# Kernel optimization log

Measured on AMD Instinct MI355X. Metric: run time of the kernel, lower is better.

## Reference

```python
import jax, jax.numpy as jnp
import numpy as np

ALPHA = 0.2  # leaky relu slope
NEG_BIG = -9000000000000000.0


def setup_inputs() -> dict:
    key = jax.random.key(0)
    k1, k2, k3, k4 = jax.random.split(key, 4)
    B, N, Fin, Fout = 8, 2048, 256, 256
    h = jax.random.normal(k1, (B, N, Fin), dtype=jnp.float32)
    adj = jax.random.randint(k2, (B, N, N), 0, 2, dtype=jnp.int32)
    # xavier_uniform with gain=1.414
    gain = 1.414
    limW = gain * np.sqrt(6.0 / (Fin + Fout))
    W = jax.random.uniform(k3, (Fin, Fout), dtype=jnp.float32, minval=-limW, maxval=limW)
    lima = gain * np.sqrt(6.0 / (2 * Fout + 1))
    a = jax.random.uniform(k4, (2 * Fout, 1), dtype=jnp.float32, minval=-lima, maxval=lima)
    return {"h": h, "adj": adj, "W": W, "a": a}


def reference(h, adj, W, a):
    # Wh: [B, N, F]
    Wh = jnp.matmul(h, W)
    Fout = W.shape[1]
    a1 = a[:Fout, 0]   # scores for source node i (repeat_interleave side)
    a2 = a[Fout:, 0]   # scores for target node j (repeat side)
    # e[b,i,j] = leakyrelu(Wh[b,i]@a1 + Wh[b,j]@a2)  -- decomposed, no O(N^2 * 2F) tensor
    s1 = jnp.einsum('bnf,f->bn', Wh, a1)  # [B, N]
    s2 = jnp.einsum('bnf,f->bn', Wh, a2)  # [B, N]
    e = jax.nn.leaky_relu(s1[:, :, None] + s2[:, None, :], negative_slope=ALPHA)
    masked = jnp.where(adj > 0, e, jnp.full_like(e, NEG_BIG))
    attention = jax.nn.softmax(masked, axis=2)  # dropout=0 (eval mode)
    h_prime = jnp.matmul(attention, Wh)  # [B, N, F]
    return jax.nn.elu(h_prime)
```

## Files before the change

kernel.cpp:

```cpp
#include <hip/hip_runtime.h>

typedef __attribute__((ext_vector_type(8))) short bhalf8;
typedef __attribute__((ext_vector_type(4))) float floatx4;

#define ALPHA_LR 0.2f

__device__ __forceinline__ unsigned short f2bf(float f) {
  union { float f; unsigned int u; } v; v.f = f;
  unsigned int r = v.u + 0x7fffu + ((v.u >> 16) & 1u);
  return (unsigned short)(r >> 16);
}
__device__ __forceinline__ float bf2f(unsigned short u) {
  union { unsigned int u; float f; } v; v.u = ((unsigned int)u) << 16;
  return v.f;
}
__device__ __forceinline__ void gld16(const void* g, void* l) {
  __builtin_amdgcn_global_load_lds((const __attribute__((address_space(1))) unsigned int*)g,
                                   (__attribute__((address_space(3))) unsigned int*)l,
                                   16, 0, 0);
}

__global__ void k0w_split(const float* __restrict__ W,
                          unsigned short* __restrict__ WThi,
                          unsigned short* __restrict__ WTlo) {
  __shared__ float s[16][17];
  const int tx = threadIdx.x, ty = threadIdx.y;
  const int n0 = blockIdx.x * 16, k0 = blockIdx.y * 16;
  s[ty][tx] = W[(k0 + ty) * 256 + n0 + tx];
  __syncthreads();
  float v = s[tx][ty];
  const int k = k0 + tx, n = n0 + ty;
  unsigned short hi = f2bf(v);
  unsigned short lo = f2bf(v - bf2f(hi));
  const int idx = (k >> 5) * 8192 + n * 32 + (k & 31);
  WThi[idx] = hi;
  WTlo[idx] = lo;
}

__global__ __launch_bounds__(512, 2) void k1_mfma(const float* __restrict__ h,
                                                  const unsigned short* __restrict__ Bhi_g,
                                                  const unsigned short* __restrict__ Blo_g,
                                                  const float* __restrict__ a_g,
                                                  unsigned short* __restrict__ WhPack,
                                                  float* __restrict__ s1,
                                                  float* __restrict__ s2) {
  __shared__ unsigned short Ah[64 * 264], Al[64 * 264];
  __shared__ unsigned short Bh[2][8192], Bl[2][8192];
  __shared__ float s1red[64], s2red[64];
  const int t = threadIdx.x;
  const long r0 = (long)blockIdx.x * 64;
  const int wave = t >> 6, lane = t & 63;

  if (t < 64) { s1red[t] = 0.f; s2red[t] = 0.f; }

#pragma unroll
  for (int rep = 0; rep < 2; rep++) {
    const int off = wave * 1024 + rep * 512;
    gld16(Bhi_g + off + lane * 8, &Bh[0][off]);
    gld16(Blo_g + off + lane * 8, &Bl[0][off]);
  }

#pragma unroll
  for (int q = 0; q < 8; q++) {
    int idx = q * 512 + t;
    int row = idx >> 6, c4 = idx & 63;
    float4 x = *(const float4*)(h + (r0 + row) * 256 + c4 * 4);
    float xs[4] = {x.x, x.y, x.z, x.w};
    unsigned short hs[4], ls[4];
#pragma unroll
    for (int qq = 0; qq < 4; qq++) {
      hs[qq] = f2bf(xs[qq]);
      ls[qq] = f2bf(xs[qq] - bf2f(hs[qq]));
    }
    *(ushort4*)&Ah[row * 264 + c4 * 4] = (ushort4){hs[0], hs[1], hs[2], hs[3]};
    *(ushort4*)&Al[row * 264 + c4 * 4] = (ushort4){ls[0], ls[1], ls[2], ls[3]};
  }
  __syncthreads();

  const int wm = wave >> 2, wn = wave & 3;
  const int lhi = lane >> 4, llo = lane & 15;

  floatx4 acc[2][4];
#pragma unroll
  for (int mt = 0; mt < 2; mt++)
#pragma unroll
    for (int nt = 0; nt < 4; nt++) acc[mt][nt] = (floatx4){0.f, 0.f, 0.f, 0.f};

  for (int ks = 0; ks < 8; ks++) {
    const int cur = ks & 1, nxt = cur ^ 1, ksn = (ks + 1) & 7;
#pragma unroll
    for (int rep = 0; rep < 2; rep++) {
      const int off = wave * 1024 + rep * 512;
      gld16(Bhi_g + ksn * 8192 + off + lane * 8, &Bh[nxt][off]);
      gld16(Blo_g + ksn * 8192 + off + lane * 8, &Bl[nxt][off]);
    }

    const int k0 = ks * 32;
    bhalf8 ah[2], al[2], bh[4], bl[4];
#pragma unroll
    for (int mt = 0; mt < 2; mt++) {
      int ro = (wm * 32 + mt * 16 + llo) * 264 + k0 + lhi * 8;
      ah[mt] = *(const bhalf8*)&Ah[ro];
      al[mt] = *(const bhalf8*)&Al[ro];
    }
#pragma unroll
    for (int nt = 0; nt < 4; nt++) {
      int ro = (wn * 64 + nt * 16 + llo) * 32 + lhi * 8;
      bh[nt] = *(const bhalf8*)&Bh[cur][ro];
      bl[nt] = *(const bhalf8*)&Bl[cur][ro];
    }
#pragma unroll
    for (int mt = 0; mt < 2; mt++)
#pragma unroll
      for (int nt = 0; nt < 4; nt++) {
        acc[mt][nt] = __builtin_amdgcn_mfma_f32_16x16x32_bf16(ah[mt], bh[nt], acc[mt][nt], 0, 0, 0);
        acc[mt][nt] = __builtin_amdgcn_mfma_f32_16x16x32_bf16(ah[mt], bl[nt], acc[mt][nt], 0, 0, 0);
        acc[mt][nt] = __builtin_amdgcn_mfma_f32_16x16x32_bf16(al[mt], bh[nt], acc[mt][nt], 0, 0, 0);
      }
    __syncthreads();
  }

  float a1v[4], a2v[4];
#pragma unroll
  for (int nt = 0; nt < 4; nt++) {
    int f = wn * 64 + nt * 16 + llo;
    a1v[nt] = a_g[f];
    a2v[nt] = a_g[256 + f];
  }

  const int b = (int)(r0 >> 11);
  const int jt_base = (int)((r0 & 2047) >> 5);

#pragma unroll
  for (int mt = 0; mt < 2; mt++) {
    float p1[4], p2[4];
#pragma unroll
    for (int reg = 0; reg < 4; reg++) {
      p1[reg] = acc[mt][0][reg] * a1v[0] + acc[mt][1][reg] * a1v[1] +
                acc[mt][2][reg] * a1v[2] + acc[mt][3][reg] * a1v[3];
      p2[reg] = acc[mt][0][reg] * a2v[0] + acc[mt][1][reg] * a2v[1] +
                acc[mt][2][reg] * a2v[2] + acc[mt][3][reg] * a2v[3];
    }
#pragma unroll
    for (int off = 1; off < 16; off <<= 1) {
#pragma unroll
      for (int reg = 0; reg < 4; reg++) {
        p1[reg] += __shfl_xor(p1[reg], off);
        p2[reg] += __shfl_xor(p2[reg], off);
      }
    }
    if (llo == 0) {
#pragma unroll
      for (int reg = 0; reg < 4; reg++) {
        int il = wm * 32 + mt * 16 + lhi * 4 + reg;
        atomicAdd(&s1red[il], p1[reg]);
        atomicAdd(&s2red[il], p2[reg]);
      }
    }
#pragma unroll
    for (int nt = 0; nt < 4; nt++) {
      int f = wn * 64 + nt * 16 + llo;
      int jt = jt_base + wm;
      ushort4 pk = (ushort4){f2bf(acc[mt][nt][0]), f2bf(acc[mt][nt][1]),
                             f2bf(acc[mt][nt][2]), f2bf(acc[mt][nt][3])};
      *(ushort4*)&WhPack[((long)((b * 64 + jt) * 256 + f)) * 32 + mt * 16 + lhi * 4] = pk;
    }
  }

  __syncthreads();
  if (t < 64) {
    s1[r0 + t] = s1red[t];
    s2[r0 + t] = s2red[t];
  }
}

__global__ __launch_bounds__(256) void k2_stats(const int* __restrict__ adj,
                                                const float* __restrict__ s1,
                                                const float* __restrict__ s2,
                                                float* __restrict__ Mv,
                                                float* __restrict__ linv,
                                                unsigned int* __restrict__ packed) {
  const int t = threadIdx.x;
  const long r = blockIdx.x;
  const int b = (int)(r >> 11);
  __shared__ float red[4];
  __shared__ int redi[4];
  __shared__ unsigned char bytes[256];

  const int4* arow = (const int4*)(adj + r * 2048);
  int4 a0 = arow[t * 2], a1 = arow[t * 2 + 1];
  unsigned int m8 = (unsigned)(a0.x > 0) | ((unsigned)(a0.y > 0) << 1) |
                    ((unsigned)(a0.z > 0) << 2) | ((unsigned)(a0.w > 0) << 3) |
                    ((unsigned)(a1.x > 0) << 4) | ((unsigned)(a1.y > 0) << 5) |
                    ((unsigned)(a1.z > 0) << 6) | ((unsigned)(a1.w > 0) << 7);

  int cnt = __popc(m8);
  for (int o = 32; o; o >>= 1) cnt += __shfl_xor(cnt, o);
  if ((t & 63) == 0) redi[t >> 6] = cnt;
  __syncthreads();
  int total = redi[0] + redi[1] + redi[2] + redi[3];
  if (total == 0) m8 = 0xFFu;

  const float4* s2p = (const float4*)(s2 + (long)b * 2048);
  float4 v0 = s2p[t * 2], v1 = s2p[t * 2 + 1];
  float sv[8] = {v0.x, v0.y, v0.z, v0.w, v1.x, v1.y, v1.z, v1.w};

  float mx = -INFINITY;
#pragma unroll
  for (int q = 0; q < 8; q++)
    if ((m8 >> q) & 1) mx = fmaxf(mx, sv[q]);
  for (int o = 32; o; o >>= 1) mx = fmaxf(mx, __shfl_xor(mx, o));
  if ((t & 63) == 0) red[t >> 6] = mx;
  __syncthreads();
  mx = fmaxf(fmaxf(red[0], red[1]), fmaxf(red[2], red[3]));

  const float s1i = s1[r];
  const float xm = s1i + mx;
  const float M = fmaxf(xm, ALPHA_LR * xm);

  float lsum = 0.f;
#pragma unroll
  for (int q = 0; q < 8; q++) {
    if ((m8 >> q) & 1) {
      float x = s1i + sv[q];
      float le = fmaxf(x, ALPHA_LR * x);
      lsum += __expf(le - M);
    }
  }
  for (int o = 32; o; o >>= 1) lsum += __shfl_xor(lsum, o);
  __syncthreads();
  if ((t & 63) == 0) red[t >> 6] = lsum;
  __syncthreads();
  lsum = red[0] + red[1] + red[2] + red[3];

  if (t == 0) { Mv[r] = M; linv[r] = 1.f / lsum; }

  bytes[t] = (unsigned char)m8;
  __syncthreads();
  if (t < 64) {
    unsigned int w = (unsigned)bytes[t * 4] | ((unsigned)bytes[t * 4 + 1] << 8) |
                     ((unsigned)bytes[t * 4 + 2] << 16) | ((unsigned)bytes[t * 4 + 3] << 24);
    packed[r * 64 + t] = w;
  }
}

__global__ __launch_bounds__(256, 3) void k3_attn(const unsigned short* __restrict__ WhPack,
                                                  const unsigned int* __restrict__ packed,
                                                  const float* __restrict__ s1g,
                                                  const float* __restrict__ s2g,
                                                  const float* __restrict__ Mg,
                                                  const float* __restrict__ lg,
                                                  float* __restrict__ out) {
  const int t = threadIdx.x;
  const int fc = blockIdx.x;
  const int ry = blockIdx.y;
  const int b = blockIdx.z;
  const int rowbase = ry * 128;

  __shared__ float s2all[2048];
  __shared__ unsigned int bits[128 * 68];
  __shared__ float lvv[128];

  {
    const float4* src = (const float4*)(s2g + (long)b * 2048);
    float4* dst = (float4*)s2all;
    dst[t] = src[t];
    dst[256 + t] = src[256 + t];
  }
  {
    const int4* src = (const int4*)(packed + ((long)b * 2048 + rowbase) * 64);
#pragma unroll
    for (int q = 0; q < 8; q++) {
      int idx = q * 256 + t;
      int row = idx >> 4, c = idx & 15;
      int4 v = src[idx];
      *(int4*)&bits[row * 68 + c * 4] = v;
    }
  }
  if (t < 128) lvv[t] = lg[(long)b * 2048 + rowbase + t];

  const int wave = t >> 6, lane = t & 63;
  const int lhi = lane >> 4, llo = lane & 15;
  const int wrow = wave * 32;

  float s1i[2], Mi[2];
#pragma unroll
  for (int mt = 0; mt < 2; mt++) {
    long r = (long)b * 2048 + rowbase + wrow + mt * 16 + llo;
    s1i[mt] = s1g[r];
    Mi[mt] = Mg[r];
  }
  __syncthreads();

  const unsigned short* Bl = WhPack + (long)b * 64 * 8192 + fc * 64 * 32 + llo * 32 + lhi * 8;

  floatx4 acc[2][4];
#pragma unroll
  for (int mt = 0; mt < 2; mt++)
#pragma unroll
    for (int nt = 0; nt < 4; nt++) acc[mt][nt] = (floatx4){0.f, 0.f, 0.f, 0.f};

  bhalf8 B0[4], B1[4];
#pragma unroll
  for (int nt = 0; nt < 4; nt++) B0[nt] = *(const bhalf8*)(Bl + nt * 512);

#define K3_STEP(JT, BUF)                                                        \
  {                                                                             \
    const int jt_ = (JT);                                                       \
    float4 s2lo = *(const float4*)&s2all[jt_ * 32 + lhi * 8];                   \
    float4 s2hi = *(const float4*)&s2all[jt_ * 32 + lhi * 8 + 4];               \
    float s2v[8] = {s2lo.x, s2lo.y, s2lo.z, s2lo.w,                             \
                    s2hi.x, s2hi.y, s2hi.z, s2hi.w};                            \
    bhalf8 afr[2];                                                              \
    _Pragma("unroll") for (int mt = 0; mt < 2; mt++) {                          \
      unsigned int wv = bits[(wrow + mt * 16 + llo) * 68 + jt_];                \
      union { unsigned int u[4]; bhalf8 v; } au;                                \
      _Pragma("unroll") for (int pp = 0; pp < 4; pp++) {                        \
        float x0 = ((wv >> (lhi * 8 + 2 * pp)) & 1u) ? (s1i[mt] + s2v[2 * pp])  \
                                                     : -1e30f;                  \
        float x1 = ((wv >> (lhi * 8 + 2 * pp + 1)) & 1u)                        \
                       ? (s1i[mt] + s2v[2 * pp + 1]) : -1e30f;                  \
        x0 = fmaxf(x0, ALPHA_LR * x0);                                          \
        x1 = fmaxf(x1, ALPHA_LR * x1);                                          \
        union { float f; unsigned int u; } u0, u1;                              \
        u0.f = __expf(x0 - Mi[mt]);                                             \
        u1.f = __expf(x1 - Mi[mt]);                                             \
        au.u[pp] = (u0.u >> 16) | (u1.u & 0xffff0000u);                         \
      }                                                                         \
      afr[mt] = au.v;                                                           \
    }                                                                           \
    _Pragma("unroll") for (int mt = 0; mt < 2; mt++)                            \
        _Pragma("unroll") for (int nt = 0; nt < 4; nt++)                        \
            acc[mt][nt] = __builtin_amdgcn_mfma_f32_16x16x32_bf16(              \
                afr[mt], BUF[nt], acc[mt][nt], 0, 0, 0);                        \
  }

  for (int jt = 0; jt < 64; jt += 2) {
    const unsigned short* p1 = Bl + (jt + 1) * 8192;
#pragma unroll
    for (int nt = 0; nt < 4; nt++) B1[nt] = *(const bhalf8*)(p1 + nt * 512);
    K3_STEP(jt, B0)
    const int jn = (jt + 2 < 64) ? jt + 2 : 63;
    const unsigned short* p0 = Bl + jn * 8192;
#pragma unroll
    for (int nt = 0; nt < 4; nt++) B0[nt] = *(const bhalf8*)(p0 + nt * 512);
    K3_STEP(jt + 1, B1)
  }
#undef K3_STEP

#pragma unroll
  for (int mt = 0; mt < 2; mt++) {
#pragma unroll
    for (int nt = 0; nt < 4; nt++) {
#pragma unroll
      for (int reg = 0; reg < 4; reg++) {
        int brow = wrow + mt * 16 + lhi * 4 + reg;
        float v = acc[mt][nt][reg] * lvv[brow];
        v = v > 0.f ? v : expm1f(v);
        out[((long)b * 2048 + rowbase + brow) * 256 + fc * 64 + nt * 16 + llo] = v;
      }
    }
  }
}

extern "C" void kernel_launch(void* const* d_in, const int* in_sizes, int n_in,
                              void* d_out, int out_size, void* d_ws, size_t ws_size,
                              hipStream_t stream) {
  const float* h = (const float*)d_in[0];
  const int* adj = (const int*)d_in[1];
  const float* W = (const float*)d_in[2];
  const float* a = (const float*)d_in[3];
  float* out = (float*)d_out;

  char* ws = (char*)d_ws;
  unsigned short* WhPack = (unsigned short*)ws;
  unsigned int* packed = (unsigned int*)(ws + 8388608);
  unsigned short* WThi = (unsigned short*)(ws + 12582912);
  unsigned short* WTlo = (unsigned short*)(ws + 12713984);
  float* s1 = (float*)(ws + 12845056);
  float* s2 = (float*)(ws + 12910592);
  float* Mv = (float*)(ws + 12976128);
  float* linv = (float*)(ws + 13041664);

  hipLaunchKernelGGL(k0w_split, dim3(16, 16), dim3(16, 16), 0, stream, W, WThi, WTlo);
  hipLaunchKernelGGL(k1_mfma, dim3(256), dim3(512), 0, stream, h, WThi, WTlo, a,
                     WhPack, s1, s2);
  hipLaunchKernelGGL(k2_stats, dim3(16384), dim3(256), 0, stream, adj, s1, s2, Mv, linv, packed);
  hipLaunchKernelGGL(k3_attn, dim3(4, 16, 8), dim3(256), 0, stream, WhPack, packed,
                     s1, s2, Mv, linv, out);
}
```

Baseline: 270.5 us.

## Materialize normalized bf16 attention matrix in stats kernel, make attn a plain GEMM

The stats kernel now computes the masked, normalized softmax probabilities once and writes them as a full bf16 matrix. The attention kernel becomes a plain bf16 MFMA GEMM that loads A fragments directly from global memory. This removes the per-element exp and mask work that was repeated across the four feature-chunk blocks, along with the LDS staging of s2 and the mask bits. In exchange it adds a 64MB intermediate write and repeated reads of it, making the kernel more memory-bound, and k3 occupancy is lowered to 2.

```diff
diff --git a/kernel.cpp b/kernel.cpp
--- a/kernel.cpp
+++ b/kernel.cpp
@@ -177,15 +177,12 @@
 __global__ __launch_bounds__(256) void k2_stats(const int* __restrict__ adj,
                                                 const float* __restrict__ s1,
                                                 const float* __restrict__ s2,
-                                                float* __restrict__ Mv,
-                                                float* __restrict__ linv,
-                                                unsigned int* __restrict__ packed) {
+                                                unsigned short* __restrict__ Pn) {
   const int t = threadIdx.x;
   const long r = blockIdx.x;
   const int b = (int)(r >> 11);
   __shared__ float red[4];
   __shared__ int redi[4];
-  __shared__ unsigned char bytes[256];
 
   const int4* arow = (const int4*)(adj + r * 2048);
   int4 a0 = arow[t * 2], a1 = arow[t * 2 + 1];
@@ -218,146 +215,85 @@
   const float xm = s1i + mx;
   const float M = fmaxf(xm, ALPHA_LR * xm);
 
+  float pq[8];
   float lsum = 0.f;
 #pragma unroll
   for (int q = 0; q < 8; q++) {
-    if ((m8 >> q) & 1) {
-      float x = s1i + sv[q];
-      float le = fmaxf(x, ALPHA_LR * x);
-      lsum += __expf(le - M);
-    }
+    float x = s1i + sv[q];
+    float le = fmaxf(x, ALPHA_LR * x);
+    float e = ((m8 >> q) & 1) ? __expf(le - M) : 0.f;
+    pq[q] = e;
+    lsum += e;
   }
   for (int o = 32; o; o >>= 1) lsum += __shfl_xor(lsum, o);
   __syncthreads();
   if ((t & 63) == 0) red[t >> 6] = lsum;
   __syncthreads();
   lsum = red[0] + red[1] + red[2] + red[3];
-
-  if (t == 0) { Mv[r] = M; linv[r] = 1.f / lsum; }
-
-  bytes[t] = (unsigned char)m8;
-  __syncthreads();
-  if (t < 64) {
-    unsigned int w = (unsigned)bytes[t * 4] | ((unsigned)bytes[t * 4 + 1] << 8) |
-                     ((unsigned)bytes[t * 4 + 2] << 16) | ((unsigned)bytes[t * 4 + 3] << 24);
-    packed[r * 64 + t] = w;
-  }
-}
-
-__global__ __launch_bounds__(256, 3) void k3_attn(const unsigned short* __restrict__ WhPack,
-                                                  const unsigned int* __restrict__ packed,
-                                                  const float* __restrict__ s1g,
-                                                  const float* __restrict__ s2g,
-                                                  const float* __restrict__ Mg,
-                                                  const float* __restrict__ lg,
+  const float linv = 1.f / lsum;
+
+  unsigned short pb[8];
+#pragma unroll
+  for (int q = 0; q < 8; q++) pb[q] = f2bf(pq[q] * linv);
+  *(int4*)&Pn[r * 2048 + t * 8] = *(const int4*)pb;
+}
+
+__global__ __launch_bounds__(256, 2) void k3_attn(const unsigned short* __restrict__ WhPack,
+                                                  const unsigned short* __restrict__ Pn,
                                                   float* __restrict__ out) {
   const int t = threadIdx.x;
   const int fc = blockIdx.x;
   const int ry = blockIdx.y;
   const int b = blockIdx.z;
-  const int rowbase = ry * 128;
-
-  __shared__ float s2all[2048];
-  __shared__ unsigned int bits[128 * 68];
-  __shared__ float lvv[128];
-
-  {
-    const float4* src = (const float4*)(s2g + (long)b * 2048);
-    float4* dst = (float4*)s2all;
-    dst[t] = src[t];
-    dst[256 + t] = src[256 + t];
-  }
-  {
-    const int4* src = (const int4*)(packed + ((long)b * 2048 + rowbase) * 64);
-#pragma unroll
-    for (int q = 0; q < 8; q++) {
-      int idx = q * 256 + t;
-      int row = idx >> 4, c = idx & 15;
-      int4 v = src[idx];
-      *(int4*)&bits[row * 68 + c * 4] = v;
-    }
-  }
-  if (t < 128) lvv[t] = lg[(long)b * 2048 + rowbase + t];
-
   const int wave = t >> 6, lane = t & 63;
   const int lhi = lane >> 4, llo = lane & 15;
-  const int wrow = wave * 32;
-
-  float s1i[2], Mi[2];
+  const int rowbase = ry * 128 + wave * 32;
+
+  const unsigned short* Bp = WhPack + ((long)b * 64) * 8192 + fc * 2048 + llo * 32 + lhi * 8;
+  const unsigned short* Ap = Pn + ((long)b * 2048 + rowbase + llo) * 2048 + lhi * 8;
+
+  floatx4 acc[2][4];
+#pragma unroll
+  for (int mt = 0; mt < 2; mt++)
+#pragma unroll
+    for (int nt = 0; nt < 4; nt++) acc[mt][nt] = (floatx4){0.f, 0.f, 0.f, 0.f};
+
+  bhalf8 A0[2], A1[2], B0[4], B1[4];
+
+#define K3_LD(AB, BB, JT)                                                     \
+  {                                                                           \
+    _Pragma("unroll") for (int mt = 0; mt < 2; mt++)                          \
+        AB[mt] = *(const bhalf8*)(Ap + mt * 32768 + (JT) * 32);               \
+    _Pragma("unroll") for (int nt = 0; nt < 4; nt++)                          \
+        BB[nt] = *(const bhalf8*)(Bp + (JT) * 8192 + nt * 512);               \
+  }
+#define K3_MM(AB, BB)                                                         \
+  _Pragma("unroll") for (int mt = 0; mt < 2; mt++)                            \
+      _Pragma("unroll") for (int nt = 0; nt < 4; nt++)                        \
+          acc[mt][nt] = __builtin_amdgcn_mfma_f32_16x16x32_bf16(              \
+              AB[mt], BB[nt], acc[mt][nt], 0, 0, 0);
+
+  K3_LD(A0, B0, 0)
+  for (int jt = 0; jt < 64; jt += 2) {
+    K3_LD(A1, B1, jt + 1)
+    K3_MM(A0, B0)
+    const int jn = (jt + 2 < 64) ? jt + 2 : 63;
+    K3_LD(A0, B0, jn)
+    K3_MM(A1, B1)
+  }
+#undef K3_LD
+#undef K3_MM
+
 #pragma unroll
   for (int mt = 0; mt < 2; mt++) {
-    long r = (long)b * 2048 + rowbase + wrow + mt * 16 + llo;
-    s1i[mt] = s1g[r];
-    Mi[mt] = Mg[r];
-  }
-  __syncthreads();
-
-  const unsigned short* Bl = WhPack + (long)b * 64 * 8192 + fc * 64 * 32 + llo * 32 + lhi * 8;
-
-  floatx4 acc[2][4];
-#pragma unroll
-  for (int mt = 0; mt < 2; mt++)
-#pragma unroll
-    for (int nt = 0; nt < 4; nt++) acc[mt][nt] = (floatx4){0.f, 0.f, 0.f, 0.f};
-
-  bhalf8 B0[4], B1[4];
-#pragma unroll
-  for (int nt = 0; nt < 4; nt++) B0[nt] = *(const bhalf8*)(Bl + nt * 512);
-
-#define K3_STEP(JT, BUF)                                                        \
-  {                                                                             \
-    const int jt_ = (JT);                                                       \
-    float4 s2lo = *(const float4*)&s2all[jt_ * 32 + lhi * 8];                   \
-    float4 s2hi = *(const float4*)&s2all[jt_ * 32 + lhi * 8 + 4];               \
-    float s2v[8] = {s2lo.x, s2lo.y, s2lo.z, s2lo.w,                             \
-                    s2hi.x, s2hi.y, s2hi.z, s2hi.w};                            \
-    bhalf8 afr[2];                                                              \
-    _Pragma("unroll") for (int mt = 0; mt < 2; mt++) {                          \
-      unsigned int wv = bits[(wrow + mt * 16 + llo) * 68 + jt_];                \
-      union { unsigned int u[4]; bhalf8 v; } au;                                \
-      _Pragma("unroll") for (int pp = 0; pp < 4; pp++) {                        \
-        float x0 = ((wv >> (lhi * 8 + 2 * pp)) & 1u) ? (s1i[mt] + s2v[2 * pp])  \
-                                                     : -1e30f;                  \
-        float x1 = ((wv >> (lhi * 8 + 2 * pp + 1)) & 1u)                        \
-                       ? (s1i[mt] + s2v[2 * pp + 1]) : -1e30f;                  \
-        x0 = fmaxf(x0, ALPHA_LR * x0);                                          \
-        x1 = fmaxf(x1, ALPHA_LR * x1);                                          \
-        union { float f; unsigned int u; } u0, u1;                              \
-        u0.f = __expf(x0 - Mi[mt]);                                             \
-        u1.f = __expf(x1 - Mi[mt]);                                             \
-        au.u[pp] = (u0.u >> 16) | (u1.u & 0xffff0000u);                         \
-      }                                                                         \
-      afr[mt] = au.v;                                                           \
-    }                                                                           \
-    _Pragma("unroll") for (int mt = 0; mt < 2; mt++)                            \
-        _Pragma("unroll") for (int nt = 0; nt < 4; nt++)                        \
-            acc[mt][nt] = __builtin_amdgcn_mfma_f32_16x16x32_bf16(              \
-                afr[mt], BUF[nt], acc[mt][nt], 0, 0, 0);                        \
-  }
-
-  for (int jt = 0; jt < 64; jt += 2) {
-    const unsigned short* p1 = Bl + (jt + 1) * 8192;
-#pragma unroll
-    for (int nt = 0; nt < 4; nt++) B1[nt] = *(const bhalf8*)(p1 + nt * 512);
-    K3_STEP(jt, B0)
-    const int jn = (jt + 2 < 64) ? jt + 2 : 63;
-    const unsigned short* p0 = Bl + jn * 8192;
-#pragma unroll
-    for (int nt = 0; nt < 4; nt++) B0[nt] = *(const bhalf8*)(p0 + nt * 512);
-    K3_STEP(jt + 1, B1)
-  }
-#undef K3_STEP
-
-#pragma unroll
-  for (int mt = 0; mt < 2; mt++) {
 #pragma unroll
     for (int nt = 0; nt < 4; nt++) {
 #pragma unroll
       for (int reg = 0; reg < 4; reg++) {
-        int brow = wrow + mt * 16 + lhi * 4 + reg;
-        float v = acc[mt][nt][reg] * lvv[brow];
+        int row = rowbase + mt * 16 + lhi * 4 + reg;
+        float v = acc[mt][nt][reg];
         v = v > 0.f ? v : expm1f(v);
-        out[((long)b * 2048 + rowbase + brow) * 256 + fc * 64 + nt * 16 + llo] = v;
+        out[((long)b * 2048 + row) * 256 + fc * 64 + nt * 16 + llo] = v;
       }
     }
   }
@@ -374,18 +310,15 @@
 
   char* ws = (char*)d_ws;
   unsigned short* WhPack = (unsigned short*)ws;
-  unsigned int* packed = (unsigned int*)(ws + 8388608);
-  unsigned short* WThi = (unsigned short*)(ws + 12582912);
-  unsigned short* WTlo = (unsigned short*)(ws + 12713984);
-  float* s1 = (float*)(ws + 12845056);
-  float* s2 = (float*)(ws + 12910592);
-  float* Mv = (float*)(ws + 12976128);
-  float* linv = (float*)(ws + 13041664);
+  unsigned short* Pn = (unsigned short*)(ws + 8388608);
+  unsigned short* WThi = (unsigned short*)(ws + 75497472);
+  unsigned short* WTlo = (unsigned short*)(ws + 75628544);
+  float* s1 = (float*)(ws + 75759616);
+  float* s2 = (float*)(ws + 75825152);
 
   hipLaunchKernelGGL(k0w_split, dim3(16, 16), dim3(16, 16), 0, stream, W, WThi, WTlo);
   hipLaunchKernelGGL(k1_mfma, dim3(256), dim3(512), 0, stream, h, WThi, WTlo, a,
                      WhPack, s1, s2);
-  hipLaunchKernelGGL(k2_stats, dim3(16384), dim3(256), 0, stream, adj, s1, s2, Mv, linv, packed);
-  hipLaunchKernelGGL(k3_attn, dim3(4, 16, 8), dim3(256), 0, stream, WhPack, packed,
-                     s1, s2, Mv, linv, out);
-}
+  hipLaunchKernelGGL(k2_stats, dim3(16384), dim3(256), 0, stream, adj, s1, s2, Pn);
+  hipLaunchKernelGGL(k3_attn, dim3(4, 16, 8), dim3(256), 0, stream, WhPack, Pn, out);
+}
```

New measurement: 290.8 us. 1.07x slower.
